# Optimization experiments

Hardware: AMD Instinct MI355X
Metric: run time of the kernel (lower is better)

The kernel has to match this reference:

```python
import jax, jax.numpy as jnp
import numpy as np

N = 50000
E = 800000
NFEAT = 128
NHID = 32
HEADS = 8
NCLASS = 40


def _gat_conv(x, src, dst, W, att_src, att_dst, bias, concat):
    # x: [N, Fin]; W: [Fin, H*C]; att_*: [H, C]; bias: [H*C] or [C]
    n = x.shape[0]
    H, C = att_src.shape
    h = (x @ W).reshape(n, H, C)                      # [N,H,C]
    a_src = (h * att_src[None]).sum(-1)               # [N,H]
    a_dst = (h * att_dst[None]).sum(-1)               # [N,H]
    e = jax.nn.leaky_relu(a_src[src] + a_dst[dst], 0.2)  # [E,H]
    # edge softmax over incoming edges of each dst node
    m = jax.ops.segment_max(e, dst, num_segments=n)   # [N,H]
    e = jnp.exp(e - m[dst])
    s = jax.ops.segment_sum(e, dst, num_segments=n)   # [N,H]
    alpha = e / (s[dst] + 1e-16)                      # [E,H]
    msg = h[src] * alpha[:, :, None]                  # [E,H,C]
    out = jax.ops.segment_sum(msg, dst, num_segments=n)  # [N,H,C]
    if concat:
        out = out.reshape(n, H * C)
    else:
        out = out.mean(axis=1)
    return out + bias


def setup_inputs() -> dict:
    key = jax.random.key(0)
    ks = jax.random.split(key, 10)
    x = jax.random.normal(ks[0], (N, NFEAT), dtype=jnp.float32)
    edge_index = jax.random.randint(ks[1], (2, E), 0, N, dtype=jnp.int64)
    sc = 1.0 / np.sqrt(NFEAT)
    W1 = jax.random.uniform(ks[2], (NFEAT, HEADS * NHID), jnp.float32, -sc, sc)
    a1_src = jax.random.uniform(ks[3], (HEADS, NHID), jnp.float32, -sc, sc)
    a1_dst = jax.random.uniform(ks[4], (HEADS, NHID), jnp.float32, -sc, sc)
    b1 = jnp.zeros((HEADS * NHID,), jnp.float32)
    sc2 = 1.0 / np.sqrt(HEADS * NHID)
    W2 = jax.random.uniform(ks[5], (HEADS * NHID, NCLASS), jnp.float32, -sc2, sc2)
    a2_src = jax.random.uniform(ks[6], (1, NCLASS), jnp.float32, -sc2, sc2)
    a2_dst = jax.random.uniform(ks[7], (1, NCLASS), jnp.float32, -sc2, sc2)
    b2 = jnp.zeros((NCLASS,), jnp.float32)
    return {"x": x, "edge_index": edge_index, "W1": W1, "a1_src": a1_src,
            "a1_dst": a1_dst, "b1": b1, "W2": W2, "a2_src": a2_src,
            "a2_dst": a2_dst, "b2": b2}


def reference(x, edge_index, W1, a1_src, a1_dst, b1, W2, a2_src, a2_dst, b2):
    n = x.shape[0]
    loop = jnp.arange(n, dtype=edge_index.dtype)
    src = jnp.concatenate([edge_index[0], loop])  # add self-loops (PyG default)
    dst = jnp.concatenate([edge_index[1], loop])
    # dropout layers are identity in eval mode
    h = jax.nn.elu(_gat_conv(x, src, dst, W1, a1_src, a1_dst, b1, concat=True))
    out = _gat_conv(h, src, dst, W2, a2_src, a2_dst, b2, concat=False)
    return jax.nn.log_softmax(out, axis=1)
```

## Files before the change

kernel.cpp:

```cpp
#include <hip/hip_runtime.h>
#include <math.h>

#define NFEAT  128
#define HC     256
#define HEADS  8
#define NHID   32
#define NCLASS 40

#define INV_LN2 1.44269504088896340736f

typedef unsigned int  uint;
typedef unsigned short ushort;
typedef unsigned char uchar;

typedef __attribute__((ext_vector_type(8))) short bf16x8;
typedef __attribute__((ext_vector_type(4))) float f32x4;

union U8 { uint4 u; bf16x8 v; };

__device__ __forceinline__ uint f2bf1(float f) {
    uint b = __float_as_uint(f);
    b += 0x7FFFu + ((b >> 16) & 1u);
    return b >> 16;
}
__device__ __forceinline__ uint packbf(float lo, float hi) {
    return f2bf1(lo) | (f2bf1(hi) << 16);
}

__device__ __forceinline__ uchar f2fp8(float v) {
    return (uchar)(__builtin_amdgcn_cvt_pk_fp8_f32(v, v, 0, false) & 0xFF);
}
__device__ __forceinline__ float fp8tof(uint byte) {
    auto v2 = __builtin_amdgcn_cvt_pk_f32_fp8((int)byte, false);
    return v2[0];
}

__device__ __forceinline__ float bperm(int addr, float v) {
    return __int_as_float(__builtin_amdgcn_ds_bpermute(addr, __float_as_int(v)));
}


#define HU 8
#define PREPB 23
__global__ __launch_bounds__(256)
void k_hist_prep(const int* __restrict__ dst, int E, int* deg,
                 int* __restrict__ rank,
                 const float* __restrict__ W1,
                 const float* __restrict__ attS, const float* __restrict__ attD,
                 const float* __restrict__ W2,
                 const float* __restrict__ a2sw, const float* __restrict__ a2dw,
                 ushort* __restrict__ Wb1, ushort* __restrict__ Wb2) {
    int blk = blockIdx.x;
    int t = threadIdx.x;
    if (blk >= PREPB) {
        int tid = (blk - PREPB) * 256 + t;
        int stride = (gridDim.x - PREPB) * 256;
#pragma unroll
        for (int j = 0; j < HU; ++j) {
            int i = tid + j * stride;
            if (i < E) rank[i] = atomicAdd(&deg[dst[i]], 1);
        }
        return;
    }
    float f[8];
    if (blk < 17) {
        int g = blk * 256 + t;
        int lane = g & 63;
        int step = (g >> 6) & 3;
        int tile = g >> 8;
        int k0 = step * 32 + (lane >> 4) * 8;
        if (tile < 16) {
            int ncol = tile * 16 + (lane & 15);
#pragma unroll
            for (int j = 0; j < 8; ++j) f[j] = W1[(size_t)(k0 + j) * HC + ncol];
        } else {
            int cc = lane & 15;
            int h = cc & 7;
            const float* av = (cc < 8) ? attS : attD;
#pragma unroll
            for (int j = 0; j < 8; ++j) {
                const float* wr = W1 + (size_t)(k0 + j) * HC + h * 32;
                float s = 0.f;
#pragma unroll
                for (int c = 0; c < 32; ++c) s += wr[c] * av[h * 32 + c];
                f[j] = s * INV_LN2;
            }
        }
        uint4 o;
        o.x = packbf(f[0], f[1]);
        o.y = packbf(f[2], f[3]);
        o.z = packbf(f[4], f[5]);
        o.w = packbf(f[6], f[7]);
        *(uint4*)(Wb1 + (size_t)g * 8) = o;
    } else {
        int g = (blk - 17) * 256 + t;
        if (g >= 3 * 8 * 64) return;
        int lane = g & 63;
        int ks = (g >> 6) & 7;
        int nt = g >> 9;
        int cc = lane & 15;
        int ncol = nt * 16 + cc;
        int k0 = ks * 32 + (lane >> 4) * 8;
        if (ncol < NCLASS) {
#pragma unroll
            for (int j = 0; j < 8; ++j) f[j] = W2[(size_t)(k0 + j) * NCLASS + ncol];
        } else if (ncol <= 41) {
            const float* av = (ncol == 40) ? a2sw : a2dw;
#pragma unroll
            for (int j = 0; j < 8; ++j) {
                const float* wr = W2 + (size_t)(k0 + j) * NCLASS;
                float s = 0.f;
#pragma unroll
                for (int c = 0; c < NCLASS; ++c) s += wr[c] * av[c];
                f[j] = s * INV_LN2;
            }
        } else {
#pragma unroll
            for (int j = 0; j < 8; ++j) f[j] = 0.f;
        }
        uint4 o;
        o.x = packbf(f[0], f[1]);
        o.y = packbf(f[2], f[3]);
        o.z = packbf(f[4], f[5]);
        o.w = packbf(f[6], f[7]);
        *(uint4*)(Wb2 + (size_t)g * 8) = o;
    }
}

#define SU 4
__global__ __launch_bounds__(256)
void k_scatter_gemm1(const int* __restrict__ srcE, const int* __restrict__ dstE,
                     const int* __restrict__ rank, int E,
                     int* __restrict__ srcs, int scb,
                     const float* __restrict__ x, const ushort* __restrict__ Wb,
                     int n, uchar* __restrict__ h1f8, float* __restrict__ a1x) {
    __shared__ uint Xs[64 * 68];
    int t = threadIdx.x;
    if (blockIdx.x < scb) {
        int tid = blockIdx.x * 256 + t;
        int stride = scb * 256;
        int P = (E + 3) >> 2;
#pragma unroll
        for (int g = 0; g < SU; ++g) {
            int pk = tid + g * stride;
            if (pk >= P) continue;
            int i0 = pk * 4;
            if (i0 + 4 <= E) {
                int4 d4 = *(const int4*)(dstE + i0);
                int4 r4 = *(const int4*)(rank + i0);
                int4 s4 = *(const int4*)(srcE + i0);
                if (r4.x < 64) srcs[((size_t)d4.x << 6) + r4.x] = s4.x;
                if (r4.y < 64) srcs[((size_t)d4.y << 6) + r4.y] = s4.y;
                if (r4.z < 64) srcs[((size_t)d4.z << 6) + r4.z] = s4.z;
                if (r4.w < 64) srcs[((size_t)d4.w << 6) + r4.w] = s4.w;
            } else {
                for (int i = i0; i < E; ++i) {
                    int r = rank[i];
                    if (r < 64) srcs[((size_t)dstE[i] << 6) + r] = srcE[i];
                }
            }
        }
        return;
    }
    int lane = t & 63;
    int w = t >> 6;
    int n0 = (blockIdx.x - scb) * 64;

#pragma unroll
    for (int j = 0; j < 8; ++j) {
        int f4 = t + j * 256;
        int node = f4 >> 5;
        int k4 = (f4 & 31) * 4;
        int gn = n0 + node;
        float4 v = make_float4(0.f, 0.f, 0.f, 0.f);
        if (gn < n) v = *(const float4*)(x + (size_t)gn * NFEAT + k4);
        uint2 pk;
        pk.x = packbf(v.x, v.y);
        pk.y = packbf(v.z, v.w);
        *(uint2*)(Xs + node * 68 + (k4 >> 1)) = pk;
    }
    __syncthreads();

    int m = lane & 15;
    int q4 = (lane >> 4) * 4;
    bf16x8 Af[4];
#pragma unroll
    for (int ks = 0; ks < 4; ++ks) {
        U8 a;
        a.u = *(const uint4*)(Xs + (w * 16 + m) * 68 + ks * 16 + q4);
        Af[ks] = a.v;
    }
    __syncthreads();

    f32x4 acc[17];
#pragma unroll
    for (int i = 0; i < 17; ++i) acc[i] = (f32x4){0.f, 0.f, 0.f, 0.f};

    const bf16x8* Bf = (const bf16x8*)Wb;
#pragma unroll
    for (int ks = 0; ks < 4; ++ks) {
#pragma unroll
        for (int nt = 0; nt < 17; ++nt) {
            bf16x8 bv = Bf[(size_t)(nt * 4 + ks) * 64 + lane];
            acc[nt] = __builtin_amdgcn_mfma_f32_16x16x32_bf16(Af[ks], bv, acc[nt], 0, 0, 0);
        }
    }

    int cc = lane & 15;
    int r0 = (lane >> 4) * 4;

#pragma unroll
    for (int r = 0; r < 4; ++r) {
        int gn = n0 + w * 16 + r0 + r;
        if (gn < n) a1x[(size_t)gn * 16 + cc] = acc[16][r];
    }

    uchar* CsB = (uchar*)Xs;
#pragma unroll
    for (int nt = 0; nt < 16; ++nt) {
#pragma unroll
        for (int r = 0; r < 4; ++r)
            CsB[(w * 16 + r0 + r) * 272 + nt * 16 + cc] = f2fp8(acc[nt][r]);
    }
    __syncthreads();

    int node_local = t >> 2;
    int q = t & 3;
    int gn = n0 + node_local;
    if (gn < n) {
        const uchar* crow = CsB + node_local * 272 + q * 64;
        uchar* hp = h1f8 + (size_t)gn * HC + q * 64;
#pragma unroll
        for (int i = 0; i < 4; ++i)
            *(uint4*)(hp + i * 16) = *(const uint4*)(crow + i * 16);
    }
}

__global__ __launch_bounds__(256)
void k_agg1(const uint* __restrict__ h1u, const float* __restrict__ a1x,
            const float* __restrict__ b1, const int* __restrict__ deg,
            const int* __restrict__ srcs,
            int n, ushort* __restrict__ hgb) {
    int wid = blockIdx.x * 4 + (threadIdx.x >> 6);
    if (wid >= n) return;
    wid = __builtin_amdgcn_readfirstlane(wid);
    int lane = threadIdx.x & 63;
    int vj = lane >> 3;
    int hh = lane & 7;
    int hacc = lane >> 3;
    float adn = a1x[(size_t)wid * 16 + 8 + hh];
    const char* a1xb = (const char*)a1x;
    int ax8  = (lane ^ 8)  << 2;
    int ax16 = (lane ^ 16) << 2;
    int ax32 = (lane ^ 32) << 2;
    int bpc  = hacc << 2;
    int bpp[8];
#pragma unroll
    for (int j = 0; j < 8; ++j) bpp[j] = ((j << 3) + hacc) << 2;

    int degw = __builtin_amdgcn_readfirstlane(deg[wid]);
    degw = (degw < 63) ? degw : 63;
    int cnt = degw + 1;
    const int* srow = srcs + ((size_t)wid << 6);

    float s = 0.f;
    float4 acc = make_float4(0.f, 0.f, 0.f, 0.f);

    for (int i = 0; i < cnt; i += 8) {
        int idx = i + vj;
        int ldi = (idx < degw) ? idx : 0;
        int lv = srow[ldi];
        int sv = (idx < degw) ? lv : wid;
        bool valid = idx < cnt;
        float av = *(const float*)(a1xb + ((size_t)(uint)sv << 6) + ((uint)hh << 2));
        float a = av + adn;
        float e = fmaxf(a, 0.2f * a);
        float p = valid ? __builtin_exp2f(e) : 0.f;
        s += p;
#pragma unroll
        for (int j = 0; j < 8; ++j) {
            int snj = srow[i + j];
            snj = ((i + j) < degw) ? snj : wid;
            uint hv = h1u[(size_t)snj * 64 + lane];
            float pj = bperm(bpp[j], p);
            auto lo = __builtin_amdgcn_cvt_pk_f32_fp8((int)hv, false);
            auto hi = __builtin_amdgcn_cvt_pk_f32_fp8((int)hv, true);
            acc.x += pj * lo[0];
            acc.y += pj * lo[1];
            acc.z += pj * hi[0];
            acc.w += pj * hi[1];
        }
    }

    float ps = s + bperm(ax8, s);
    ps += bperm(ax16, ps);
    ps += bperm(ax32, ps);
    float inv = 1.f / (ps + 1e-16f);
    float inv_a = bperm(bpc, inv);
    float4 bv = *(const float4*)(b1 + lane * 4);
    float4 o;
    o.x = acc.x * inv_a + bv.x;
    o.y = acc.y * inv_a + bv.y;
    o.z = acc.z * inv_a + bv.z;
    o.w = acc.w * inv_a + bv.w;
    o.x = (o.x > 0.f) ? o.x : (__expf(o.x) - 1.f);
    o.y = (o.y > 0.f) ? o.y : (__expf(o.y) - 1.f);
    o.z = (o.z > 0.f) ? o.z : (__expf(o.z) - 1.f);
    o.w = (o.w > 0.f) ? o.w : (__expf(o.w) - 1.f);
    uint2 ov;
    ov.x = packbf(o.x, o.y);
    ov.y = packbf(o.z, o.w);
    *(uint2*)(hgb + (size_t)wid * HC + lane * 4) = ov;
}

__global__ __launch_bounds__(256)
void k_gemm2(const ushort* __restrict__ hgb, const ushort* __restrict__ Wb2,
             int n, uchar* __restrict__ h2f8) {
    __shared__ uint Xs[64 * 132];
    int t = threadIdx.x;
    int lane = t & 63;
    int w = t >> 6;
    int n0 = blockIdx.x * 64;

#pragma unroll
    for (int j = 0; j < 8; ++j) {
        int g = t + j * 256;
        int node = g >> 5;
        int u4 = g & 31;
        int gn = n0 + node;
        uint4 v = make_uint4(0u, 0u, 0u, 0u);
        if (gn < n) v = *(const uint4*)(hgb + (size_t)gn * HC + u4 * 8);
        *(uint4*)(Xs + node * 132 + u4 * 4) = v;
    }
    __syncthreads();

    int m = lane & 15;
    int q4 = (lane >> 4) * 4;
    bf16x8 Af[8];
#pragma unroll
    for (int ks = 0; ks < 8; ++ks) {
        U8 a;
        a.u = *(const uint4*)(Xs + (w * 16 + m) * 132 + ks * 16 + q4);
        Af[ks] = a.v;
    }
    __syncthreads();

    f32x4 acc[3];
#pragma unroll
    for (int i = 0; i < 3; ++i) acc[i] = (f32x4){0.f, 0.f, 0.f, 0.f};

    const bf16x8* Bf = (const bf16x8*)Wb2;
#pragma unroll
    for (int ks = 0; ks < 8; ++ks) {
#pragma unroll
        for (int nt = 0; nt < 3; ++nt) {
            bf16x8 bv = Bf[(size_t)(nt * 8 + ks) * 64 + lane];
            acc[nt] = __builtin_amdgcn_mfma_f32_16x16x32_bf16(Af[ks], bv, acc[nt], 0, 0, 0);
        }
    }

    int cc = lane & 15;
    int r0 = (lane >> 4) * 4;

    uchar* CsB = (uchar*)Xs;
#pragma unroll
    for (int nt = 0; nt < 2; ++nt) {
#pragma unroll
        for (int r = 0; r < 4; ++r)
            CsB[(w * 16 + r0 + r) * 64 + nt * 16 + cc] = f2fp8(acc[nt][r]);
    }
#pragma unroll
    for (int r = 0; r < 4; ++r) {
        int row = (w * 16 + r0 + r) * 64;
        if (cc < 8)       CsB[row + 32 + cc] = f2fp8(acc[2][r]);
        else if (cc == 8) *(float*)(CsB + row + 40) = acc[2][r];
        else if (cc == 9) *(float*)(CsB + row + 44) = acc[2][r];
        else if (cc == 10) *(uint*)(CsB + row + 48) = 0u;
        else if (cc == 11) *(uint*)(CsB + row + 52) = 0u;
        else if (cc == 12) *(uint*)(CsB + row + 56) = 0u;
        else if (cc == 13) *(uint*)(CsB + row + 60) = 0u;
    }
    __syncthreads();

    int node_local = t >> 2;
    int q = t & 3;
    int gn = n0 + node_local;
    if (gn < n)
        *(uint4*)(h2f8 + (size_t)gn * 64 + q * 16) =
            *(const uint4*)(CsB + node_local * 64 + q * 16);
}

__global__ __launch_bounds__(256)
void k_agg2(const uchar* __restrict__ h2f8, const float* __restrict__ b2,
            const int* __restrict__ deg, const int* __restrict__ srcs,
            int n, float* __restrict__ out) {
    int wid = blockIdx.x * 4 + (threadIdx.x >> 6);
    if (wid >= n) return;
    wid = __builtin_amdgcn_readfirstlane(wid);
    int lane = threadIdx.x & 63;
    int vj = lane & 7;
    bool live = lane < NCLASS;
    int col = live ? lane : 0;
    const char* h2b = (const char*)h2f8;
    float adn = *(const float*)(h2b + (size_t)wid * 64 + 44);
    int ax1 = (lane ^ 1) << 2;
    int ax2 = (lane ^ 2) << 2;
    int ax4 = (lane ^ 4) << 2;
    int bpj[8];
#pragma unroll
    for (int j = 0; j < 8; ++j) bpj[j] = j << 2;

    int degw = __builtin_amdgcn_readfirstlane(deg[wid]);
    degw = (degw < 63) ? degw : 63;
    int cnt = degw + 1;
    const int* srow = srcs + ((size_t)wid << 6);

    float s = 0.f, acc = 0.f;

    for (int i = 0; i < cnt; i += 8) {
        int idx = i + vj;
        int ldi = (idx < degw) ? idx : 0;
        int lv = srow[ldi];
        int sv = (idx < degw) ? lv : wid;
        bool valid = idx < cnt;
        float av = *(const float*)(h2b + ((size_t)(uint)sv << 6) + 40u);
        float a = av + adn;
        float e = fmaxf(a, 0.2f * a);
        float p = valid ? __builtin_exp2f(e) : 0.f;
        s += p;
#pragma unroll
        for (int j = 0; j < 8; ++j) {
            int snj = srow[i + j];
            snj = ((i + j) < degw) ? snj : wid;
            uint hb = h2f8[(size_t)snj * 64 + col];
            float pj = bperm(bpj[j], p);
            acc += pj * fp8tof(hb);
        }
    }

    float ps = s + bperm(ax1, s);
    ps += bperm(ax2, ps);
    ps += bperm(ax4, ps);

    float val0 = acc / (ps + 1e-16f) + (live ? b2[lane] : 0.f);
    float vmax = live ? val0 : -INFINITY;
#pragma unroll
    for (int msk = 1; msk < 64; msk <<= 1) vmax = fmaxf(vmax, __shfl_xor(vmax, msk, 64));
    float ex = live ? __expf(val0 - vmax) : 0.f;
#pragma unroll
    for (int msk = 1; msk < 64; msk <<= 1) ex += __shfl_xor(ex, msk, 64);
    float res = val0 - vmax - __logf(ex);
    if (live) out[(size_t)wid * NCLASS + lane] = res;
}

extern "C" void kernel_launch(void* const* d_in, const int* in_sizes, int n_in,
                              void* d_out, int out_size, void* d_ws, size_t ws_size,
                              hipStream_t stream) {
    const float* x    = (const float*)d_in[0];
    const int*   ei   = (const int*)  d_in[1];
    const float* W1   = (const float*)d_in[2];
    const float* attS = (const float*)d_in[3];
    const float* attD = (const float*)d_in[4];
    const float* b1   = (const float*)d_in[5];
    const float* W2   = (const float*)d_in[6];
    const float* a2sw = (const float*)d_in[7];
    const float* a2dw = (const float*)d_in[8];
    const float* b2   = (const float*)d_in[9];

    int n = in_sizes[0] / NFEAT;
    int E = in_sizes[1] / 2;
    const int* srcE = ei;
    const int* dstE = ei + E;
    int mblocks = (n + 63) / 64;

    char* p = (char*)d_ws;
    auto alloc = [&](size_t bytes) {
        char* r = p;
        p += (bytes + 255) & ~(size_t)255;
        return r;
    };
    uchar*  h1f8 = (uchar*)alloc((size_t)n * HC);
    ushort* hgb  = (ushort*)alloc((size_t)n * HC * 2);
    uchar*  h2f8 = (uchar*)alloc((size_t)n * 64);
    ushort* Wb1  = (ushort*)alloc((size_t)17 * 4 * 64 * 8 * 2);
    ushort* Wb2  = (ushort*)alloc((size_t)3 * 8 * 64 * 8 * 2);
    float* a1x = (float*)alloc((size_t)n * 16 * 4);
    int* deg  = (int*)alloc((size_t)n * 4);
    int* rank = (int*)alloc((size_t)E * 4);
    int* srcs = (int*)alloc((size_t)n * 64 * 4);

    int histb = (E + 256 * HU - 1) / (256 * HU);
    int P = (E + 3) / 4;
    int scb = (P + 256 * SU - 1) / (256 * SU);
    hipMemsetAsync(deg, 0, (size_t)n * 4, stream);
    k_hist_prep<<<PREPB + histb, 256, 0, stream>>>(dstE, E, deg, rank,
                                                   W1, attS, attD, W2, a2sw, a2dw,
                                                   Wb1, Wb2);
    k_scatter_gemm1<<<scb + mblocks, 256, 0, stream>>>(
        srcE, dstE, rank, E, srcs, scb, x, Wb1, n, h1f8, a1x);
    k_agg1<<<(n + 3) / 4, 256, 0, stream>>>((const uint*)h1f8, a1x, b1,
                                            deg, srcs, n, hgb);
    k_gemm2<<<mblocks, 256, 0, stream>>>(hgb, Wb2, n, h2f8);
    k_agg2<<<(n + 3) / 4, 256, 0, stream>>>(h2f8, b2, deg, srcs, n, (float*)d_out);
}
```

Measured before the change: 230.2 us.

## Double-buffer neighbor gathers and broadcast source indices via lane ops

Both aggregation kernels now load the node's whole source-index row once into a register (one per lane). Each chunk's indices are then distributed with bpermute and readlane instead of repeated global loads. The edge loop is software-pipelined with two chunk buffers, so the gathers for the next 8 neighbors are issued before the current chunk is consumed. This targets gather latency and redundant index loads, at the cost of more registers per thread and possibly lower occupancy.

```diff
diff --git a/kernel.cpp b/kernel.cpp
--- a/kernel.cpp
+++ b/kernel.cpp
@@ -37,6 +37,9 @@
 
 __device__ __forceinline__ float bperm(int addr, float v) {
     return __int_as_float(__builtin_amdgcn_ds_bpermute(addr, __float_as_int(v)));
+}
+__device__ __forceinline__ int bperm_i(int addr, int v) {
+    return __builtin_amdgcn_ds_bpermute(addr, v);
 }
 
 
@@ -261,36 +264,64 @@
     int degw = __builtin_amdgcn_readfirstlane(deg[wid]);
     degw = (degw < 63) ? degw : 63;
     int cnt = degw + 1;
-    const int* srow = srcs + ((size_t)wid << 6);
+    int sv_full = srcs[((size_t)wid << 6) + lane];
 
     float s = 0.f;
     float4 acc = make_float4(0.f, 0.f, 0.f, 0.f);
 
-    for (int i = 0; i < cnt; i += 8) {
-        int idx = i + vj;
-        int ldi = (idx < degw) ? idx : 0;
-        int lv = srow[ldi];
-        int sv = (idx < degw) ? lv : wid;
-        bool valid = idx < cnt;
-        float av = *(const float*)(a1xb + ((size_t)(uint)sv << 6) + ((uint)hh << 2));
-        float a = av + adn;
-        float e = fmaxf(a, 0.2f * a);
-        float p = valid ? __builtin_exp2f(e) : 0.f;
-        s += p;
-#pragma unroll
-        for (int j = 0; j < 8; ++j) {
-            int snj = srow[i + j];
-            snj = ((i + j) < degw) ? snj : wid;
-            uint hv = h1u[(size_t)snj * 64 + lane];
-            float pj = bperm(bpp[j], p);
-            auto lo = __builtin_amdgcn_cvt_pk_f32_fp8((int)hv, false);
-            auto hi = __builtin_amdgcn_cvt_pk_f32_fp8((int)hv, true);
-            acc.x += pj * lo[0];
-            acc.y += pj * lo[1];
-            acc.z += pj * hi[0];
-            acc.w += pj * hi[1];
-        }
-    }
+    struct Chunk { float av; uint hv[8]; };
+    Chunk A, B;
+
+#define LOADC1(C, base) do {                                                   \
+    int idxl_ = (base) + vj;                                                   \
+    int svv_ = bperm_i(idxl_ << 2, sv_full);                                   \
+    svv_ = (idxl_ < degw) ? svv_ : wid;                                        \
+    (C).av = *(const float*)(a1xb + ((size_t)(uint)svv_ << 6) + ((uint)hh << 2)); \
+    _Pragma("unroll")                                                          \
+    for (int j_ = 0; j_ < 8; ++j_) {                                           \
+        int sn_ = __builtin_amdgcn_readlane(sv_full, (base) + j_);             \
+        sn_ = (((base) + j_) < degw) ? sn_ : wid;                              \
+        (C).hv[j_] = h1u[(size_t)(uint)sn_ * 64 + lane];                       \
+    }                                                                          \
+} while (0)
+
+#define CONSC1(C, base) do {                                                   \
+    int idxl_ = (base) + vj;                                                   \
+    float a_ = (C).av + adn;                                                   \
+    float e_ = fmaxf(a_, 0.2f * a_);                                           \
+    float p_ = (idxl_ < cnt) ? __builtin_exp2f(e_) : 0.f;                      \
+    s += p_;                                                                   \
+    _Pragma("unroll")                                                          \
+    for (int j_ = 0; j_ < 8; ++j_) {                                           \
+        float pj_ = bperm(bpp[j_], p_);                                        \
+        auto lo_ = __builtin_amdgcn_cvt_pk_f32_fp8((int)(C).hv[j_], false);    \
+        auto hi_ = __builtin_amdgcn_cvt_pk_f32_fp8((int)(C).hv[j_], true);     \
+        acc.x += pj_ * lo_[0];                                                 \
+        acc.y += pj_ * lo_[1];                                                 \
+        acc.z += pj_ * hi_[0];                                                 \
+        acc.w += pj_ * hi_[1];                                                 \
+    }                                                                          \
+} while (0)
+
+    int i = 0;
+    LOADC1(A, 0);
+    while (i + 8 < cnt) {
+        LOADC1(B, i + 8);
+        CONSC1(A, i);
+        i += 8;
+        if (i + 8 < cnt) {
+            LOADC1(A, i + 8);
+            CONSC1(B, i);
+            i += 8;
+        } else {
+            CONSC1(B, i);
+            goto tail1;
+        }
+    }
+    CONSC1(A, i);
+tail1:;
+#undef LOADC1
+#undef CONSC1
 
     float ps = s + bperm(ax8, s);
     ps += bperm(ax16, ps);
@@ -413,30 +444,58 @@
     int degw = __builtin_amdgcn_readfirstlane(deg[wid]);
     degw = (degw < 63) ? degw : 63;
     int cnt = degw + 1;
-    const int* srow = srcs + ((size_t)wid << 6);
+    int sv_full = srcs[((size_t)wid << 6) + lane];
 
     float s = 0.f, acc = 0.f;
 
-    for (int i = 0; i < cnt; i += 8) {
-        int idx = i + vj;
-        int ldi = (idx < degw) ? idx : 0;
-        int lv = srow[ldi];
-        int sv = (idx < degw) ? lv : wid;
-        bool valid = idx < cnt;
-        float av = *(const float*)(h2b + ((size_t)(uint)sv << 6) + 40u);
-        float a = av + adn;
-        float e = fmaxf(a, 0.2f * a);
-        float p = valid ? __builtin_exp2f(e) : 0.f;
-        s += p;
-#pragma unroll
-        for (int j = 0; j < 8; ++j) {
-            int snj = srow[i + j];
-            snj = ((i + j) < degw) ? snj : wid;
-            uint hb = h2f8[(size_t)snj * 64 + col];
-            float pj = bperm(bpj[j], p);
-            acc += pj * fp8tof(hb);
-        }
-    }
+    struct Chunk2 { float av; uint hb[8]; };
+    Chunk2 A, B;
+
+#define LOADC2(C, base) do {                                                   \
+    int idxl_ = (base) + vj;                                                   \
+    int svv_ = bperm_i(idxl_ << 2, sv_full);                                   \
+    svv_ = (idxl_ < degw) ? svv_ : wid;                                        \
+    (C).av = *(const float*)(h2b + ((size_t)(uint)svv_ << 6) + 40u);           \
+    _Pragma("unroll")                                                          \
+    for (int j_ = 0; j_ < 8; ++j_) {                                           \
+        int sn_ = __builtin_amdgcn_readlane(sv_full, (base) + j_);             \
+        sn_ = (((base) + j_) < degw) ? sn_ : wid;                              \
+        (C).hb[j_] = h2f8[(size_t)(uint)sn_ * 64 + col];                       \
+    }                                                                          \
+} while (0)
+
+#define CONSC2(C, base) do {                                                   \
+    int idxl_ = (base) + vj;                                                   \
+    float a_ = (C).av + adn;                                                   \
+    float e_ = fmaxf(a_, 0.2f * a_);                                           \
+    float p_ = (idxl_ < cnt) ? __builtin_exp2f(e_) : 0.f;                      \
+    s += p_;                                                                   \
+    _Pragma("unroll")                                                          \
+    for (int j_ = 0; j_ < 8; ++j_) {                                           \
+        float pj_ = bperm(bpj[j_], p_);                                        \
+        acc += pj_ * fp8tof((C).hb[j_]);                                       \
+    }                                                                          \
+} while (0)
+
+    int i = 0;
+    LOADC2(A, 0);
+    while (i + 8 < cnt) {
+        LOADC2(B, i + 8);
+        CONSC2(A, i);
+        i += 8;
+        if (i + 8 < cnt) {
+            LOADC2(A, i + 8);
+            CONSC2(B, i);
+            i += 8;
+        } else {
+            CONSC2(B, i);
+            goto tail2;
+        }
+    }
+    CONSC2(A, i);
+tail2:;
+#undef LOADC2
+#undef CONSC2
 
     float ps = s + bperm(ax1, s);
     ps += bperm(ax2, ps);
```

Result: no change. 227.8 us (-1.1%).
